# Kernel tuning notes

Hardware: AMD Instinct MI355X
Metric: run time of the kernel (lower is better)

The kernel has to match this reference:

```python
import jax, jax.numpy as jnp
import numpy as np

EPS = 1e-12


def pairwise_sqdist(x, y):
    # x: (B, N, 3), y: (B, M, 3) -> (B, N, M) squared euclidean distances
    xx = jnp.sum(x * x, axis=-1)              # (B, N)
    yy = jnp.sum(y * y, axis=-1)              # (B, M)
    xy = jnp.einsum('bnd,bmd->bnm', x, y)     # (B, N, M)
    d = xx[:, :, None] + yy[None_ if False else yy[:, None, :].shape and 0 or ...] if False else xx[:, :, None] + yy[:, None, :] - 2.0 * xy
    return jnp.maximum(d, 0.0)


def chamfer_l1(x, y):
    # pytorch3d/PoinTr-style ChamferDistanceL1:
    # mean over points of sqrt(min squared dist), averaged over both directions
    d = pairwise_sqdist(x, y)                 # (B, N, M)
    d1 = jnp.min(d, axis=2)                   # (B, N) x -> nearest y
    d2 = jnp.min(d, axis=1)                   # (B, M) y -> nearest x
    d1 = jnp.sqrt(jnp.maximum(d1, EPS))
    d2 = jnp.sqrt(jnp.maximum(d2, EPS))
    return 0.5 * (jnp.mean(d1) + jnp.mean(d2))


def knn1_gather(x, y):
    # For each point in x (B,N,3), find nearest neighbor in y (B,M,3) (K=1)
    # and gather it -> (B, N, 3). Matches knn_points + knn_gather + squeeze.
    d = pairwise_sqdist(x, y)                 # (B, N, M)
    idx = jnp.argmin(d, axis=2)               # (B, N) int
    return jnp.take_along_axis(y, idx[:, :, None], axis=1)  # (B, N, 3)


def volume_with_wedge(p):
    # wedge-product volume over consecutive point triples:
    # V = sum_i (p_i x p_{i+1}) . p_{i+2} / 6  -> (B,)
    c = jnp.cross(p[:, :-2, :], p[:, 1:-1, :])  # (B, N-2, 3)
    return jnp.sum(jnp.einsum('bnd,bnd->bn', c, p[:, 2:, :]), axis=-1) / 6.0


def setup_inputs() -> dict:
    key = jax.random.key(0)
    k1, k2, k3 = jax.random.split(key, 3)
    B, Nc, Nf, M = 2, 512, 8192, 8192
    return {
        'source_coarse': jax.random.normal(k1, (B, Nc, 3), dtype=jnp.float32),
        'source_fine': jax.random.normal(k2, (B, Nf, 3), dtype=jnp.float32),
        'target_points': jax.random.normal(k3, (B, M, 3), dtype=jnp.float32),
    }


def reference(source_coarse, source_fine, target_points):
    lambda_rot = lambda_ref = lambda_align = lambda_geo = 1.0
    B = source_fine.shape[0]
    axis = jnp.broadcast_to(jnp.array([0.0, 0.0, 1.0], dtype=source_fine.dtype), (B, 3))
    plane_normal = jnp.broadcast_to(jnp.array([0.0, 1.0, 0.0], dtype=source_fine.dtype), (B, 3))

    # KNN (K=1) gather of nearest target point for each fine source point
    new_target = knn1_gather(source_fine, target_points)  # (B, Nf, 3)

    # alignment (Chamfer L1) losses
    loss_align_coarse = chamfer_l1(source_coarse, target_points)
    loss_align_fine = chamfer_l1(source_fine, target_points)

    # rotational symmetry loss
    in_proj = jnp.einsum('bij,bj->bi', source_fine, axis)      # (B, Nf)
    re_proj = jnp.einsum('bij,bj->bi', new_target, axis)
    loss_rot = jnp.mean((jnp.linalg.norm(in_proj, axis=-1) - jnp.linalg.norm(re_proj, axis=-1)) ** 2)

    # reflectional symmetry loss
    pn = plane_normal / jnp.linalg.norm(plane_normal, axis=-1, keepdims=True)
    in_dist = jnp.einsum('bij,bj->bi', source_fine, pn)
    re_dist = jnp.einsum('bij,bj->bi', new_target, pn)
    loss_ref = jnp.mean((in_dist - re_dist) ** 2)

    # geometric consistency (wedge-product volume) loss
    loss_geo = jnp.mean((volume_with_wedge(source_fine) - volume_with_wedge(new_target)) ** 2)

    total = (lambda_rot * loss_rot + lambda_ref * loss_ref
             + lambda_align * loss_align_coarse + lambda_align * loss_align_fine
             + lambda_geo * loss_geo)
    return total
```

## Files before the change

### kernel.cpp

```cpp
#include <hip/hip_runtime.h>
#include <stdint.h>
#include <float.h>

using u64 = unsigned long long;
typedef float v2f __attribute__((ext_vector_type(2)));

constexpr int B_ = 2;
constexpr int NC = 512;
constexpr int NF = 8192;
constexpr int MT = 8192;

constexpr int TPB  = 256;
constexpr int RPB  = 512;
constexpr int TILE = 256;
constexpr int CF   = 16;
constexpr int TAIL_BLOCKS = 196;

#define DEVINL __device__ __forceinline__

template<bool ARGMIN>
DEVINL void pairmin_body(const float* __restrict__ P, const float* __restrict__ Q,
                         int nP, int nQ, int b, int row_base, int j0, int ntiles,
                         int chunk, int nRowsTot,
                         u64* __restrict__ outPack, unsigned* __restrict__ outVal,
                         float4* tile)
{
#pragma clang fp contract(off)
    const int tid  = threadIdx.x;
    const int row0 = row_base + tid;
    const int row1 = row_base + tid + TPB;
    const float* p0 = P + ((size_t)b * nP + row0) * 3;
    const float* p1 = P + ((size_t)b * nP + row1) * 3;
    float a0 = p0[0], a1 = p0[1], a2 = p0[2];
    float e0 = p1[0], e1 = p1[1], e2 = p1[2];
    v2f tx0 = {2.0f * a0, 2.0f * e0};
    v2f tx1 = {2.0f * a1, 2.0f * e1};
    v2f tx2 = {2.0f * a2, 2.0f * e2};
    v2f txx = {(a0*a0 + a1*a1) + a2*a2, (e0*e0 + e1*e1) + e2*e2};
    v2f dbest = {FLT_MAX, FLT_MAX};
    const v2f vzero = {0.0f, 0.0f};
    int jb0 = 0, jb1 = 0;

    for (int t = 0; t < ntiles; ++t) {
        __syncthreads();
        {
            const float* q = Q + ((size_t)b * nQ + j0 + t * TILE + tid) * 3;
            float q0 = q[0], q1 = q[1], q2 = q[2];
            tile[tid] = make_float4(q0, q1, q2, (q0*q0 + q1*q1) + q2*q2);
        }
        __syncthreads();
        const int jbase = j0 + t * TILE;
        for (int jj = 0; jj < TILE; jj += 4) {
            float4 qv[4];
            #pragma unroll
            for (int u = 0; u < 4; ++u) qv[u] = tile[jj + u];
            #pragma unroll
            for (int u = 0; u < 4; ++u) {
                v2f s  = (tx0 * qv[u].x + tx1 * qv[u].y) + tx2 * qv[u].z;
                v2f tt = txx + qv[u].w;
                v2f d  = tt - s;
                v2f dc = __builtin_elementwise_max(d, vzero);
                if (ARGMIN) {
                    int j = jbase + jj + u;
                    bool c0 = dc.x < dbest.x;
                    dbest.x = c0 ? dc.x : dbest.x;  jb0 = c0 ? j : jb0;
                    bool c1 = dc.y < dbest.y;
                    dbest.y = c1 ? dc.y : dbest.y;  jb1 = c1 ? j : jb1;
                } else {
                    dbest = __builtin_elementwise_min(dbest, dc);
                }
            }
        }
    }
    const size_t o0 = (size_t)chunk * nRowsTot + (size_t)b * nP;
    if (ARGMIN) {
        outPack[o0 + row0] = ((u64)__float_as_uint(dbest.x) << 32) | (unsigned)jb0;
        outPack[o0 + row1] = ((u64)__float_as_uint(dbest.y) << 32) | (unsigned)jb1;
    } else {
        outVal[o0 + row0] = __float_as_uint(dbest.x);
        outVal[o0 + row1] = __float_as_uint(dbest.y);
    }
}

__global__ __launch_bounds__(TPB, 8) void pairmin_all(
    const float* __restrict__ coarse, const float* __restrict__ fine,
    const float* __restrict__ tgt,
    u64* __restrict__ pfr, unsigned* __restrict__ pfc,
    unsigned* __restrict__ pcr, unsigned* __restrict__ pcc,
    unsigned* __restrict__ counter)
{
    __shared__ float4 tile[TILE];
    const int bx = blockIdx.x;
    if (bx == 0 && threadIdx.x == 0) *counter = 0;
    if (bx < 64) {
        int chunk = bx & 31, b = bx >> 5;
        pairmin_body<false>(coarse, tgt, NC, MT, b, 0, chunk * TILE, 1,
                            chunk, B_ * NC, nullptr, pcr, tile);
    } else if (bx < 128) {
        int i = bx - 64;
        int chunk = i & 1, yb = (i >> 1) & 15, b = i >> 5;
        pairmin_body<false>(tgt, coarse, MT, NC, b, yb * RPB, chunk * TILE, 1,
                            chunk, B_ * MT, nullptr, pcc, tile);
    } else if (bx < 640) {
        int i = bx - 128;
        int chunk = i & 15, yb = (i >> 4) & 15, b = i >> 8;
        pairmin_body<true>(fine, tgt, NF, MT, b, yb * RPB, chunk * (MT / CF), 2,
                           chunk, B_ * NF, pfr, nullptr, tile);
    } else {
        int i = bx - 640;
        int chunk = i & 15, yb = (i >> 4) & 15, b = i >> 8;
        pairmin_body<false>(tgt, fine, MT, NF, b, yb * RPB, chunk * (NF / CF), 2,
                            chunk, B_ * MT, nullptr, pfc, tile);
    }
}

__global__ __launch_bounds__(TPB) void tail_all(
    const float* __restrict__ fine, const float* __restrict__ tgt,
    const u64* __restrict__ pfr, const unsigned* __restrict__ pfc,
    const unsigned* __restrict__ pcr, const unsigned* __restrict__ pcc,
    double* __restrict__ bs, unsigned* __restrict__ counter,
    float* __restrict__ out)
{
    __shared__ float sp[TPB + 2][3], yp[TPB + 2][3];
    __shared__ double redw[4][9];
    __shared__ double lred[4][13];
    __shared__ int lastflag;
    const int bx = blockIdx.x, tid = threadIdx.x;
    const int wave = tid >> 6, lane = tid & 63;

    double v_s = 0, v_d2f = 0, v_d1c = 0, v_d2c = 0, v_yd2 = 0, v_zs = 0, v_zt = 0;
    double vs = 0, vt = 0;
    int role_b = 0;

    if (bx < 64) {
        const int base = bx * TPB;
        const int g = base + tid;
        const int b = base >> 13;  role_b = b;
        u64 best = pfr[g];
        #pragma unroll
        for (int c = 1; c < CF; ++c) {
            u64 p = pfr[(size_t)c * (B_ * NF) + g];
            best = p < best ? p : best;
        }
        float d1 = __uint_as_float((unsigned)(best >> 32));
        int idx  = (int)(best & 0xffffffffULL);
        float s = sqrtf(fmaxf(d1, 1e-12f));
        const float* y  = tgt  + ((size_t)b * MT + idx) * 3;
        const float* sr = fine + (size_t)g * 3;
        float y0 = y[0],  y1 = y[1],  y2 = y[2];
        float s0 = sr[0], s1 = sr[1], s2 = sr[2];
        yp[tid][0] = y0; yp[tid][1] = y1; yp[tid][2] = y2;
        sp[tid][0] = s0; sp[tid][1] = s1; sp[tid][2] = s2;
        const int base_b = base & (NF - 1);
        if (tid < 2 && base_b + TPB + tid < NF) {
            int g2 = base + TPB + tid;
            u64 b2 = pfr[g2];
            #pragma unroll
            for (int c = 1; c < CF; ++c) {
                u64 p = pfr[(size_t)c * (B_ * NF) + g2];
                b2 = p < b2 ? p : b2;
            }
            int i2 = (int)(b2 & 0xffffffffULL);
            const float* yh = tgt  + ((size_t)b * MT + i2) * 3;
            const float* sh = fine + (size_t)g2 * 3;
            #pragma unroll
            for (int k = 0; k < 3; ++k) { yp[TPB + tid][k] = yh[k]; sp[TPB + tid][k] = sh[k]; }
        }
        __syncthreads();
        v_s = s;
        float yd = s1 - y1;
        v_yd2 = (double)(yd * yd);
        v_zs  = (double)(s2 * s2);
        v_zt  = (double)(y2 * y2);
        int rb = base_b + tid;
        if (rb <= NF - 3) {
            {
                const float* a = sp[tid]; const float* c = sp[tid+1]; const float* e = sp[tid+2];
                float c0 = a[1]*c[2] - a[2]*c[1];
                float c1 = a[2]*c[0] - a[0]*c[2];
                float c2 = a[0]*c[1] - a[1]*c[0];
                vs = (double)(c0*e[0] + c1*e[1] + c2*e[2]);
            }
            {
                const float* a = yp[tid]; const float* c = yp[tid+1]; const float* e = yp[tid+2];
                float c0 = a[1]*c[2] - a[2]*c[1];
                float c1 = a[2]*c[0] - a[0]*c[2];
                float c2 = a[0]*c[1] - a[1]*c[0];
                vt = (double)(c0*e[0] + c1*e[1] + c2*e[2]);
            }
        }
    } else if (bx < 128) {
        const int g = (bx - 64) * TPB + tid;
        unsigned best = pfc[g];
        #pragma unroll
        for (int c = 1; c < CF; ++c) best = min(best, pfc[(size_t)c * (B_ * MT) + g]);
        v_d2f = (double)sqrtf(fmaxf(__uint_as_float(best), 1e-12f));
    } else if (bx < 132) {
        const int g = (bx - 128) * TPB + tid;
        unsigned best = pcr[g];
        #pragma unroll
        for (int c = 1; c < 32; ++c) best = min(best, pcr[(size_t)c * (B_ * NC) + g]);
        v_d1c = (double)sqrtf(fmaxf(__uint_as_float(best), 1e-12f));
    } else {
        const int g = (bx - 132) * TPB + tid;
        unsigned best = min(pcc[g], pcc[(size_t)(B_ * MT) + g]);
        v_d2c = (double)sqrtf(fmaxf(__uint_as_float(best), 1e-12f));
    }

    double r9[9] = {v_s, v_d2f, v_d1c, v_d2c, v_yd2, v_zs, v_zt, vs, vt};
    for (int o = 32; o; o >>= 1) {
        #pragma unroll
        for (int k = 0; k < 9; ++k) r9[k] += __shfl_down(r9[k], o);
    }
    if (lane == 0) {
        #pragma unroll
        for (int k = 0; k < 9; ++k) redw[wave][k] = r9[k];
    }
    __syncthreads();
    if (tid == 0) {
        double t9[9];
        #pragma unroll
        for (int k = 0; k < 9; ++k)
            t9[k] = redw[0][k] + redw[1][k] + redw[2][k] + redw[3][k];
        double* o = bs + (size_t)bx * 16;
        #pragma unroll
        for (int k = 0; k < 16; ++k) o[k] = 0.0;
        o[0] = t9[0]; o[1] = t9[1]; o[2] = t9[2]; o[3] = t9[3]; o[4] = t9[4];
        o[5 + role_b]  = t9[5];
        o[7 + role_b]  = t9[6];
        o[9 + role_b]  = t9[7];
        o[11 + role_b] = t9[8];
        __threadfence();
        unsigned old = atomicAdd(counter, 1u);
        lastflag = (old == TAIL_BLOCKS - 1);
    }
    __syncthreads();
    if (!lastflag) return;

    __threadfence();
    double c13[13];
    if (tid < TAIL_BLOCKS) {
        const double* p = bs + (size_t)tid * 16;
        #pragma unroll
        for (int k = 0; k < 13; ++k) c13[k] = p[k];
    } else {
        #pragma unroll
        for (int k = 0; k < 13; ++k) c13[k] = 0.0;
    }
    for (int o = 32; o; o >>= 1) {
        #pragma unroll
        for (int k = 0; k < 13; ++k) c13[k] += __shfl_down(c13[k], o);
    }
    if (lane == 0) {
        #pragma unroll
        for (int k = 0; k < 13; ++k) lred[wave][k] = c13[k];
    }
    __syncthreads();
    if (tid == 0) {
        double S[13];
        #pragma unroll
        for (int k = 0; k < 13; ++k)
            S[k] = lred[0][k] + lred[1][k] + lred[2][k] + lred[3][k];
        double m_d1f = S[0] / (double)(B_ * NF);
        double m_d2f = S[1] / (double)(B_ * MT);
        double m_d1c = S[2] / (double)(B_ * NC);
        double m_d2c = S[3] / (double)(B_ * MT);
        double loss_align_fine   = 0.5 * (m_d1f + m_d2f);
        double loss_align_coarse = 0.5 * (m_d1c + m_d2c);
        double loss_ref = S[4] / (double)(B_ * NF);
        double loss_rot = 0.0, loss_geo = 0.0;
        for (int b = 0; b < B_; ++b) {
            double dn = sqrt(S[5 + b]) - sqrt(S[7 + b]);
            loss_rot += dn * dn;
            double dv = (S[9 + b] - S[11 + b]) / 6.0;
            loss_geo += dv * dv;
        }
        loss_rot /= (double)B_;
        loss_geo /= (double)B_;
        out[0] = (float)(loss_rot + loss_ref + loss_align_coarse + loss_align_fine + loss_geo);
    }
}

extern "C" void kernel_launch(void* const* d_in, const int* in_sizes, int n_in,
                              void* d_out, int out_size, void* d_ws, size_t ws_size,
                              hipStream_t stream)
{
    const float* src_coarse = (const float*)d_in[0];
    const float* src_fine   = (const float*)d_in[1];
    const float* tgt        = (const float*)d_in[2];
    float* out = (float*)d_out;
    char*  ws  = (char*)d_ws;

    u64*      pfr     = (u64*)(ws);
    unsigned* pfc     = (unsigned*)(ws + 2097152);
    unsigned* pcr     = (unsigned*)(ws + 3145728);
    unsigned* pcc     = (unsigned*)(ws + 3276800);
    double*   bs      = (double*)(ws + 3407872);
    unsigned* counter = (unsigned*)(ws + 3432960);

    pairmin_all<<<dim3(1152), TPB, 0, stream>>>(
        src_coarse, src_fine, tgt, pfr, pfc, pcr, pcc, counter);
    tail_all<<<dim3(TAIL_BLOCKS), TPB, 0, stream>>>(
        src_fine, tgt, pfr, pfc, pcr, pcc, bs, counter, out);
}
```

Measured before the change: 129.5 us.

## Prefetch next tile, double-buffer LDS reads, and hoist clamp out of inner loop

The next tile's global loads are issued into registers before the compute loop, so global latency overlaps with work on the current tile. LDS reads are double-buffered in groups of eight so shared-memory latency is hidden. The per-pair max-with-zero clamp moves to a single clamp of the final minimum, which is equivalent because max(·,0) is monotonic, though argmin tie-breaking among negative distances can change. Launch bounds drop from 8 to 4 waves per SIMD to make room for the extra registers, at the risk of lower occupancy.

```diff
diff --git a/kernel.cpp b/kernel.cpp
--- a/kernel.cpp
+++ b/kernel.cpp
@@ -38,51 +38,67 @@
     v2f tx2 = {2.0f * a2, 2.0f * e2};
     v2f txx = {(a0*a0 + a1*a1) + a2*a2, (e0*e0 + e1*e1) + e2*e2};
     v2f dbest = {FLT_MAX, FLT_MAX};
+    int jb0 = 0, jb1 = 0;
+
+    auto PROC = [&](const float4 qv, const int j) {
+#pragma clang fp contract(off)
+        v2f s = (tx0 * qv.x + tx1 * qv.y) + tx2 * qv.z;
+        v2f d = (txx + qv.w) - s;
+        if (ARGMIN) {
+            bool c0 = d.x < dbest.x;
+            bool c1 = d.y < dbest.y;
+            dbest = __builtin_elementwise_min(d, dbest);
+            jb0 = c0 ? j : jb0;
+            jb1 = c1 ? j : jb1;
+        } else {
+            dbest = __builtin_elementwise_min(dbest, d);
+        }
+    };
+
+    {
+        const float* q = Q + ((size_t)b * nQ + j0 + tid) * 3;
+        float nq0 = q[0], nq1 = q[1], nq2 = q[2];
+
+        for (int t = 0; t < ntiles; ++t) {
+            __syncthreads();
+            tile[tid] = make_float4(nq0, nq1, nq2, (nq0*nq0 + nq1*nq1) + nq2*nq2);
+            if (t + 1 < ntiles) {
+                const float* qn = Q + ((size_t)b * nQ + j0 + (t + 1) * TILE + tid) * 3;
+                nq0 = qn[0]; nq1 = qn[1]; nq2 = qn[2];
+            }
+            __syncthreads();
+            const int jbase = j0 + t * TILE;
+
+            float4 qa[8], qb[8];
+            #pragma unroll
+            for (int u = 0; u < 8; ++u) qa[u] = tile[u];
+
+            for (int jj = 0; jj < TILE; jj += 16) {
+                #pragma unroll
+                for (int u = 0; u < 8; ++u) qb[u] = tile[jj + 8 + u];
+                #pragma unroll
+                for (int u = 0; u < 8; ++u) PROC(qa[u], jbase + jj + u);
+                #pragma unroll
+                for (int u = 0; u < 8; ++u) qa[u] = tile[(jj + 16 + u) & (TILE - 1)];
+                #pragma unroll
+                for (int u = 0; u < 8; ++u) PROC(qb[u], jbase + jj + 8 + u);
+            }
+        }
+    }
+
     const v2f vzero = {0.0f, 0.0f};
-    int jb0 = 0, jb1 = 0;
-
-    for (int t = 0; t < ntiles; ++t) {
-        __syncthreads();
-        {
-            const float* q = Q + ((size_t)b * nQ + j0 + t * TILE + tid) * 3;
-            float q0 = q[0], q1 = q[1], q2 = q[2];
-            tile[tid] = make_float4(q0, q1, q2, (q0*q0 + q1*q1) + q2*q2);
-        }
-        __syncthreads();
-        const int jbase = j0 + t * TILE;
-        for (int jj = 0; jj < TILE; jj += 4) {
-            float4 qv[4];
-            #pragma unroll
-            for (int u = 0; u < 4; ++u) qv[u] = tile[jj + u];
-            #pragma unroll
-            for (int u = 0; u < 4; ++u) {
-                v2f s  = (tx0 * qv[u].x + tx1 * qv[u].y) + tx2 * qv[u].z;
-                v2f tt = txx + qv[u].w;
-                v2f d  = tt - s;
-                v2f dc = __builtin_elementwise_max(d, vzero);
-                if (ARGMIN) {
-                    int j = jbase + jj + u;
-                    bool c0 = dc.x < dbest.x;
-                    dbest.x = c0 ? dc.x : dbest.x;  jb0 = c0 ? j : jb0;
-                    bool c1 = dc.y < dbest.y;
-                    dbest.y = c1 ? dc.y : dbest.y;  jb1 = c1 ? j : jb1;
-                } else {
-                    dbest = __builtin_elementwise_min(dbest, dc);
-                }
-            }
-        }
-    }
+    v2f dcl = __builtin_elementwise_max(dbest, vzero);
     const size_t o0 = (size_t)chunk * nRowsTot + (size_t)b * nP;
     if (ARGMIN) {
-        outPack[o0 + row0] = ((u64)__float_as_uint(dbest.x) << 32) | (unsigned)jb0;
-        outPack[o0 + row1] = ((u64)__float_as_uint(dbest.y) << 32) | (unsigned)jb1;
+        outPack[o0 + row0] = ((u64)__float_as_uint(dcl.x) << 32) | (unsigned)jb0;
+        outPack[o0 + row1] = ((u64)__float_as_uint(dcl.y) << 32) | (unsigned)jb1;
     } else {
-        outVal[o0 + row0] = __float_as_uint(dbest.x);
-        outVal[o0 + row1] = __float_as_uint(dbest.y);
+        outVal[o0 + row0] = __float_as_uint(dcl.x);
+        outVal[o0 + row1] = __float_as_uint(dcl.y);
     }
 }
 
-__global__ __launch_bounds__(TPB, 8) void pairmin_all(
+__global__ __launch_bounds__(TPB, 4) void pairmin_all(
     const float* __restrict__ coarse, const float* __restrict__ fine,
     const float* __restrict__ tgt,
     u64* __restrict__ pfr, unsigned* __restrict__ pfc,
```

After: 127.0 us. 1.02x faster.
